# Optimization experiments

Hardware: AMD Instinct MI355X
Metric: run time of the kernel (lower is better)

The kernel has to match this reference:

```python
import jax, jax.numpy as jnp
import numpy as np

T, B, F, H, O = 512, 64, 128, 512, 16


def setup_inputs() -> dict:
    key = jax.random.key(0)
    ks = jax.random.split(key, 8)
    s = 1.0 / np.sqrt(H)  # torch RNN/Linear default uniform init scale
    u = lambda k, shape: jax.random.uniform(k, shape, jnp.float32, -s, s)
    return {
        "x_rnn": jax.random.normal(ks[0], (T, B, F), jnp.float32),
        "w_ih": u(ks[1], (3 * H, F)),   # gate order: r, z, n (PyTorch GRU)
        "w_hh": u(ks[2], (3 * H, H)),
        "b_ih": u(ks[3], (3 * H,)),
        "b_hh": u(ks[4], (3 * H,)),
        "w_out": u(ks[5], (O, H)),
        "b_out": u(ks[6], (O,)),
    }


def reference(x_rnn, w_ih, w_hh, b_ih, b_hh, w_out, b_out):
    # Single-layer GRU, seq-first (T, B, F), h0 = zeros (torch default when hx=None).
    h_dim = w_hh.shape[1]
    # Precompute all input-side gate pre-activations in one big GEMM: (T, B, 3H)
    xg = jnp.einsum("tbf,gf->tbg", x_rnn, w_ih) + b_ih

    def step(h, xg_t):
        hg = h @ w_hh.T + b_hh               # (B, 3H)
        xr, xz, xn = jnp.split(xg_t, 3, axis=-1)
        hr, hz, hn = jnp.split(hg, 3, axis=-1)
        r = jax.nn.sigmoid(xr + hr)
        z = jax.nn.sigmoid(xz + hz)
        n = jnp.tanh(xn + r * hn)
        h_new = (1.0 - z) * n + z * h
        return h_new, h_new

    h0 = jnp.zeros((x_rnn.shape[1], h_dim), x_rnn.dtype)
    _, hs = jax.lax.scan(step, h0, xg)       # hs: (T, B, H)
    # Output projection y = hs @ W_out^T + b_out -> (T, B, O)
    return jnp.einsum("tbh,oh->tbo", hs, w_out) + b_out
```

## Files before the change

### kernel.cpp

```cpp
#include <hip/hip_runtime.h>
#include <stdint.h>
#include <stddef.h>


#define T_LEN 512
#define B_SZ  64
#define F_DIM 128
#define H_DIM 512
#define O_DIM 16
#define SENTINEL 0xAAAAAAAAu

typedef __attribute__((ext_vector_type(8))) short short8;
typedef __attribute__((ext_vector_type(4))) float floatx4;
typedef __attribute__((ext_vector_type(2))) float floatx2;
typedef __attribute__((ext_vector_type(4))) unsigned int uintx4;

__device__ __forceinline__ unsigned short f2bf(float f) {
  unsigned u = __builtin_bit_cast(unsigned, f);
  u += 0x7fffu + ((u >> 16) & 1u);
  return (unsigned short)(u >> 16);
}

__device__ __forceinline__ float sigmoidf_(float x) {
  return 1.0f / (1.0f + __expf(-x));
}

__device__ __forceinline__ float tanhf_(float x) {
  float v = fminf(fmaxf(x, -10.f), 10.f);
  float e = __expf(2.f * v);
  return (e - 1.f) / (e + 1.f);
}

__device__ __forceinline__ short8 cvt8(floatx4 f0, floatx4 f1) {
  short8 a;
  a[0] = (short)f2bf(f0[0]); a[1] = (short)f2bf(f0[1]);
  a[2] = (short)f2bf(f0[2]); a[3] = (short)f2bf(f0[3]);
  a[4] = (short)f2bf(f1[0]); a[5] = (short)f2bf(f1[1]);
  a[6] = (short)f2bf(f1[2]); a[7] = (short)f2bf(f1[3]);
  return a;
}

__device__ __forceinline__ void hload4_sc1(floatx4* hf, const unsigned short* hbase) {
  asm volatile(
      "global_load_dwordx4 %0, %4, off sc1\n\t"
      "global_load_dwordx4 %1, %4, off offset:64 sc1\n\t"
      "global_load_dwordx4 %2, %4, off offset:128 sc1\n\t"
      "global_load_dwordx4 %3, %4, off offset:192 sc1\n\t"
      "s_waitcnt vmcnt(0)"
      : "=&v"(hf[0]), "=&v"(hf[1]), "=&v"(hf[2]), "=&v"(hf[3])
      : "v"(hbase)
      : "memory");
}

__global__ __launch_bounds__(256, 1)
void gru_persistent(const float* __restrict__ x,
                    const float* __restrict__ w_ih,
                    const float* __restrict__ w_hh,
                    const float* __restrict__ b_ih,
                    const float* __restrict__ b_hh,
                    unsigned short* __restrict__ hs) {
  __shared__ float part[2][4][4][16][33];

  const int tid  = threadIdx.x;
  const int lane = tid & 63;
  const int wv   = tid >> 6;
  const int bg   = blockIdx.x >> 4;
  const int cg   = blockIdx.x & 15;
  const int bgbase  = bg * 16;
  const int colbase = cg * 32;
  const int n16  = lane & 15;
  const int quad = lane >> 4;

  short8 bwx[3][2];
  short8 bwh[3][2][4];
  #pragma unroll
  for (int g = 0; g < 3; ++g) {
    #pragma unroll
    for (int nt = 0; nt < 2; ++nt) {
      const int grow = g * H_DIM + colbase + nt * 16 + n16;
      const float* pih = w_ih + (size_t)grow * F_DIM + wv * 32 + quad * 8;
      {
        short8 v;
        #pragma unroll
        for (int j = 0; j < 8; ++j) v[j] = (short)f2bf(pih[j]);
        bwx[g][nt] = v;
      }
      const float* phh = w_hh + (size_t)grow * H_DIM + wv * 128 + quad * 8;
      #pragma unroll
      for (int i = 0; i < 4; ++i) {
        short8 v;
        #pragma unroll
        for (int j = 0; j < 8; ++j) v[j] = (short)f2bf(phh[i * 32 + j]);
        bwh[g][nt][i] = v;
      }
    }
  }

  const int ew_b  = tid >> 4;
  const int ew_j0 = (tid & 15) * 2;
  float b_rz[2], b_zz[2], b_in[2], b_hn[2];
  #pragma unroll
  for (int e = 0; e < 2; ++e) {
    const int c = colbase + ew_j0 + e;
    b_rz[e] = b_ih[c] + b_hh[c];
    b_zz[e] = b_ih[H_DIM + c] + b_hh[H_DIM + c];
    b_in[e] = b_ih[2 * H_DIM + c];
    b_hn[e] = b_hh[2 * H_DIM + c];
  }
  float hm[2] = {0.0f, 0.0f};

  floatx4 xf0, xf1;
  {
    const float* px = x + ((size_t)(bgbase + n16)) * F_DIM + wv * 32 + quad * 8;
    xf0 = *(const floatx4*)px;
    xf1 = *(const floatx4*)(px + 4);
  }

  int mguard = 1 << 18;

  for (int t = 0; t < T_LEN; ++t) {
    floatx4 aR0 = {0.f,0.f,0.f,0.f}, aR1 = {0.f,0.f,0.f,0.f};
    floatx4 aZ0 = {0.f,0.f,0.f,0.f}, aZ1 = {0.f,0.f,0.f,0.f};
    floatx4 aX0 = {0.f,0.f,0.f,0.f}, aX1 = {0.f,0.f,0.f,0.f};
    floatx4 aH0 = {0.f,0.f,0.f,0.f}, aH1 = {0.f,0.f,0.f,0.f};
    {
      short8 a = cvt8(xf0, xf1);
      aR0 = __builtin_amdgcn_mfma_f32_16x16x32_bf16(a, bwx[0][0], aR0, 0, 0, 0);
      aR1 = __builtin_amdgcn_mfma_f32_16x16x32_bf16(a, bwx[0][1], aR1, 0, 0, 0);
      aZ0 = __builtin_amdgcn_mfma_f32_16x16x32_bf16(a, bwx[1][0], aZ0, 0, 0, 0);
      aZ1 = __builtin_amdgcn_mfma_f32_16x16x32_bf16(a, bwx[1][1], aZ1, 0, 0, 0);
      aX0 = __builtin_amdgcn_mfma_f32_16x16x32_bf16(a, bwx[2][0], aX0, 0, 0, 0);
      aX1 = __builtin_amdgcn_mfma_f32_16x16x32_bf16(a, bwx[2][1], aX1, 0, 0, 0);
    }

    if (t > 0) {
      floatx4 hf[4];
      {
        const unsigned short* hbase =
            hs + ((size_t)((t - 1) * B_SZ + bgbase + n16)) * H_DIM + wv * 128 + quad * 8;
        while (true) {
          hload4_sc1(hf, hbase);
          bool ok = true;
          #pragma unroll
          for (int i = 0; i < 4; ++i) {
            uintx4 u = __builtin_bit_cast(uintx4, hf[i]);
            ok = ok && (u[0] != SENTINEL) && (u[1] != SENTINEL) &&
                       (u[2] != SENTINEL) && (u[3] != SENTINEL);
          }
          if (__ballot(!ok) == 0ull) break;
          if (--mguard <= 0) break;
        }
      }
      if (t + 1 < T_LEN) {
        const float* px = x + ((size_t)((t + 1) * B_SZ + bgbase + n16)) * F_DIM +
                          wv * 32 + quad * 8;
        xf0 = *(const floatx4*)px;
        xf1 = *(const floatx4*)(px + 4);
      }
      #pragma unroll
      for (int i = 0; i < 4; ++i) {
        short8 a = __builtin_bit_cast(short8, hf[i]);
        aR0 = __builtin_amdgcn_mfma_f32_16x16x32_bf16(a, bwh[0][0][i], aR0, 0, 0, 0);
        aR1 = __builtin_amdgcn_mfma_f32_16x16x32_bf16(a, bwh[0][1][i], aR1, 0, 0, 0);
        aZ0 = __builtin_amdgcn_mfma_f32_16x16x32_bf16(a, bwh[1][0][i], aZ0, 0, 0, 0);
        aZ1 = __builtin_amdgcn_mfma_f32_16x16x32_bf16(a, bwh[1][1][i], aZ1, 0, 0, 0);
        aH0 = __builtin_amdgcn_mfma_f32_16x16x32_bf16(a, bwh[2][0][i], aH0, 0, 0, 0);
        aH1 = __builtin_amdgcn_mfma_f32_16x16x32_bf16(a, bwh[2][1][i], aH1, 0, 0, 0);
      }
    } else {
      const float* px = x + ((size_t)(B_SZ + bgbase + n16)) * F_DIM + wv * 32 + quad * 8;
      xf0 = *(const floatx4*)px;
      xf1 = *(const floatx4*)(px + 4);
    }

    {
      const int tb = t & 1;
      #pragma unroll
      for (int i = 0; i < 4; ++i) {
        const int r = quad * 4 + i;
        part[tb][wv][0][r][n16]      = aR0[i];
        part[tb][wv][0][r][16 + n16] = aR1[i];
        part[tb][wv][1][r][n16]      = aZ0[i];
        part[tb][wv][1][r][16 + n16] = aZ1[i];
        part[tb][wv][2][r][n16]      = aX0[i];
        part[tb][wv][2][r][16 + n16] = aX1[i];
        part[tb][wv][3][r][n16]      = aH0[i];
        part[tb][wv][3][r][16 + n16] = aH1[i];
      }
    }
    __syncthreads();

    {
      const int tb = t & 1;
      floatx2 pr = {0.f, 0.f}, pz = {0.f, 0.f}, pxn = {0.f, 0.f}, ph = {0.f, 0.f};
      #pragma unroll
      for (int w = 0; w < 4; ++w) {
        pr  += *(const floatx2*)&part[tb][w][0][ew_b][ew_j0];
        pz  += *(const floatx2*)&part[tb][w][1][ew_b][ew_j0];
        pxn += *(const floatx2*)&part[tb][w][2][ew_b][ew_j0];
        ph  += *(const floatx2*)&part[tb][w][3][ew_b][ew_j0];
      }
      unsigned short hb[2];
      #pragma unroll
      for (int e = 0; e < 2; ++e) {
        const float r = sigmoidf_(pr[e] + b_rz[e]);
        const float z = sigmoidf_(pz[e] + b_zz[e]);
        const float n = tanhf_(pxn[e] + b_in[e] + r * (ph[e] + b_hn[e]));
        const float hn2 = (1.0f - z) * n + z * hm[e];
        hm[e] = hn2;
        hb[e] = f2bf(hn2);
      }
      const unsigned int packed = ((unsigned int)hb[1] << 16) | (unsigned int)hb[0];
      unsigned int* dst = (unsigned int*)(hs +
          ((size_t)(t * B_SZ + bgbase + ew_b)) * H_DIM + colbase + ew_j0);
      __hip_atomic_store(dst, packed, __ATOMIC_RELAXED, __HIP_MEMORY_SCOPE_AGENT);
    }
  }
}

__global__ __launch_bounds__(256, 1)
void gru_proj(const unsigned short* __restrict__ hs,
              const float* __restrict__ w_out,
              const float* __restrict__ b_out,
              float* __restrict__ y) {
  const int tid  = threadIdx.x;
  const int lane = tid & 63;
  const int wv   = tid >> 6;
  const int n16  = lane & 15;
  const int quad = lane >> 4;
  const size_t rowbase = ((size_t)blockIdx.x * 4 + wv) * 16;

  short8 bw[16];
  const float* pw = w_out + (size_t)n16 * H_DIM + quad * 8;
  #pragma unroll
  for (int kc = 0; kc < 16; ++kc) {
    short8 v;
    #pragma unroll
    for (int j = 0; j < 8; ++j) v[j] = (short)f2bf(pw[kc * 32 + j]);
    bw[kc] = v;
  }
  const float bo = b_out[n16];

  const unsigned short* hbase = hs + (rowbase + n16) * H_DIM + quad * 8;
  floatx4 acc = {0.f, 0.f, 0.f, 0.f};
  #pragma unroll
  for (int kc = 0; kc < 16; ++kc) {
    short8 a = *(const short8*)(hbase + kc * 32);
    acc = __builtin_amdgcn_mfma_f32_16x16x32_bf16(a, bw[kc], acc, 0, 0, 0);
  }
  #pragma unroll
  for (int i = 0; i < 4; ++i) {
    const size_t r = rowbase + quad * 4 + i;
    y[r * O_DIM + n16] = acc[i] + bo;
  }
}

extern "C" void kernel_launch(void* const* d_in, const int* in_sizes, int n_in,
                              void* d_out, int out_size, void* d_ws, size_t ws_size,
                              hipStream_t stream) {
  (void)in_sizes; (void)n_in; (void)out_size; (void)ws_size;
  const float* x     = (const float*)d_in[0];
  const float* w_ih  = (const float*)d_in[1];
  const float* w_hh  = (const float*)d_in[2];
  const float* b_ih  = (const float*)d_in[3];
  const float* b_hh  = (const float*)d_in[4];
  const float* w_out = (const float*)d_in[5];
  const float* b_out = (const float*)d_in[6];
  float* y = (float*)d_out;

  unsigned short* hs = (unsigned short*)d_ws;

  gru_persistent<<<64, 256, 0, stream>>>(x, w_ih, w_hh, b_ih, b_hh, hs);
  gru_proj<<<(T_LEN * B_SZ) / 16 / 4, 256, 0, stream>>>(hs, w_out, b_out, y);
}
```

Measured before the change: 1.136 ms.

## Fuse output projection into persistent GRU kernel with concurrent consumer blocks

Merges the recurrence and output projection into one launch: 64 blocks run the GRU recurrence while 64 extra blocks poll hs for finished timesteps and apply the projection concurrently, removing the second kernel launch and its serialized tail. The recurrent loop is restructured so h loads are issued before the input-side MFMAs to hide latency, the partial-sum LDS layout is changed to interleave gates for vector reads, and divisions are replaced with rcp plus a Newton step. This relies on sentinel-based polling and on all 128 blocks being co-resident, and consumer polling adds memory traffic.

```diff
diff --git a/kernel.cpp b/kernel.cpp
--- a/kernel.cpp
+++ b/kernel.cpp
@@ -12,8 +12,9 @@
 
 typedef __attribute__((ext_vector_type(8))) short short8;
 typedef __attribute__((ext_vector_type(4))) float floatx4;
-typedef __attribute__((ext_vector_type(2))) float floatx2;
 typedef __attribute__((ext_vector_type(4))) unsigned int uintx4;
+
+#define MFMA16(a, b, c) __builtin_amdgcn_mfma_f32_16x16x32_bf16((a), (b), (c), 0, 0, 0)
 
 __device__ __forceinline__ unsigned short f2bf(float f) {
   unsigned u = __builtin_bit_cast(unsigned, f);
@@ -21,14 +22,19 @@
   return (unsigned short)(u >> 16);
 }
 
+__device__ __forceinline__ float fastrcp(float d) {
+  float r = __builtin_amdgcn_rcpf(d);
+  return r * (2.0f - d * r);
+}
+
 __device__ __forceinline__ float sigmoidf_(float x) {
-  return 1.0f / (1.0f + __expf(-x));
+  return fastrcp(1.0f + __expf(-x));
 }
 
 __device__ __forceinline__ float tanhf_(float x) {
   float v = fminf(fmaxf(x, -10.f), 10.f);
   float e = __expf(2.f * v);
-  return (e - 1.f) / (e + 1.f);
+  return (e - 1.f) * fastrcp(e + 1.f);
 }
 
 __device__ __forceinline__ short8 cvt8(floatx4 f0, floatx4 f1) {
@@ -38,6 +44,17 @@
   a[4] = (short)f2bf(f1[0]); a[5] = (short)f2bf(f1[1]);
   a[6] = (short)f2bf(f1[2]); a[7] = (short)f2bf(f1[3]);
   return a;
+}
+
+__device__ __forceinline__ void hissue4(floatx4* hf, const unsigned short* hbase) {
+  asm volatile(
+      "global_load_dwordx4 %0, %4, off sc1\n\t"
+      "global_load_dwordx4 %1, %4, off offset:64 sc1\n\t"
+      "global_load_dwordx4 %2, %4, off offset:128 sc1\n\t"
+      "global_load_dwordx4 %3, %4, off offset:192 sc1"
+      : "=&v"(hf[0]), "=&v"(hf[1]), "=&v"(hf[2]), "=&v"(hf[3])
+      : "v"(hbase)
+      : "memory");
 }
 
 __device__ __forceinline__ void hload4_sc1(floatx4* hf, const unsigned short* hbase) {
@@ -52,206 +69,254 @@
       : "memory");
 }
 
+__device__ __forceinline__ bool clean4(const floatx4* hf) {
+  bool ok = true;
+  #pragma unroll
+  for (int i = 0; i < 4; ++i) {
+    uintx4 u = __builtin_bit_cast(uintx4, hf[i]);
+    ok = ok & (u[0] != SENTINEL) & (u[1] != SENTINEL) &
+         (u[2] != SENTINEL) & (u[3] != SENTINEL);
+  }
+  return __ballot(!ok) == 0ull;
+}
+
 __global__ __launch_bounds__(256, 1)
-void gru_persistent(const float* __restrict__ x,
-                    const float* __restrict__ w_ih,
-                    const float* __restrict__ w_hh,
-                    const float* __restrict__ b_ih,
-                    const float* __restrict__ b_hh,
-                    unsigned short* __restrict__ hs) {
-  __shared__ float part[2][4][4][16][33];
-
-  const int tid  = threadIdx.x;
-  const int lane = tid & 63;
-  const int wv   = tid >> 6;
-  const int bg   = blockIdx.x >> 4;
-  const int cg   = blockIdx.x & 15;
-  const int bgbase  = bg * 16;
-  const int colbase = cg * 32;
-  const int n16  = lane & 15;
-  const int quad = lane >> 4;
-
-  short8 bwx[3][2];
-  short8 bwh[3][2][4];
-  #pragma unroll
-  for (int g = 0; g < 3; ++g) {
-    #pragma unroll
-    for (int nt = 0; nt < 2; ++nt) {
-      const int grow = g * H_DIM + colbase + nt * 16 + n16;
-      const float* pih = w_ih + (size_t)grow * F_DIM + wv * 32 + quad * 8;
-      {
-        short8 v;
-        #pragma unroll
-        for (int j = 0; j < 8; ++j) v[j] = (short)f2bf(pih[j]);
-        bwx[g][nt] = v;
-      }
-      const float* phh = w_hh + (size_t)grow * H_DIM + wv * 128 + quad * 8;
-      #pragma unroll
-      for (int i = 0; i < 4; ++i) {
-        short8 v;
-        #pragma unroll
-        for (int j = 0; j < 8; ++j) v[j] = (short)f2bf(phh[i * 32 + j]);
-        bwh[g][nt][i] = v;
-      }
-    }
-  }
-
-  const int ew_b  = tid >> 4;
-  const int ew_j0 = (tid & 15) * 2;
-  float b_rz[2], b_zz[2], b_in[2], b_hn[2];
-  #pragma unroll
-  for (int e = 0; e < 2; ++e) {
-    const int c = colbase + ew_j0 + e;
-    b_rz[e] = b_ih[c] + b_hh[c];
-    b_zz[e] = b_ih[H_DIM + c] + b_hh[H_DIM + c];
-    b_in[e] = b_ih[2 * H_DIM + c];
-    b_hn[e] = b_hh[2 * H_DIM + c];
-  }
-  float hm[2] = {0.0f, 0.0f};
-
-  floatx4 xf0, xf1;
-  {
-    const float* px = x + ((size_t)(bgbase + n16)) * F_DIM + wv * 32 + quad * 8;
-    xf0 = *(const floatx4*)px;
-    xf1 = *(const floatx4*)(px + 4);
-  }
-
-  int mguard = 1 << 18;
-
-  for (int t = 0; t < T_LEN; ++t) {
-    floatx4 aR0 = {0.f,0.f,0.f,0.f}, aR1 = {0.f,0.f,0.f,0.f};
-    floatx4 aZ0 = {0.f,0.f,0.f,0.f}, aZ1 = {0.f,0.f,0.f,0.f};
-    floatx4 aX0 = {0.f,0.f,0.f,0.f}, aX1 = {0.f,0.f,0.f,0.f};
-    floatx4 aH0 = {0.f,0.f,0.f,0.f}, aH1 = {0.f,0.f,0.f,0.f};
-    {
-      short8 a = cvt8(xf0, xf1);
-      aR0 = __builtin_amdgcn_mfma_f32_16x16x32_bf16(a, bwx[0][0], aR0, 0, 0, 0);
-      aR1 = __builtin_amdgcn_mfma_f32_16x16x32_bf16(a, bwx[0][1], aR1, 0, 0, 0);
-      aZ0 = __builtin_amdgcn_mfma_f32_16x16x32_bf16(a, bwx[1][0], aZ0, 0, 0, 0);
-      aZ1 = __builtin_amdgcn_mfma_f32_16x16x32_bf16(a, bwx[1][1], aZ1, 0, 0, 0);
-      aX0 = __builtin_amdgcn_mfma_f32_16x16x32_bf16(a, bwx[2][0], aX0, 0, 0, 0);
-      aX1 = __builtin_amdgcn_mfma_f32_16x16x32_bf16(a, bwx[2][1], aX1, 0, 0, 0);
-    }
-
-    if (t > 0) {
-      floatx4 hf[4];
-      {
-        const unsigned short* hbase =
-            hs + ((size_t)((t - 1) * B_SZ + bgbase + n16)) * H_DIM + wv * 128 + quad * 8;
-        while (true) {
-          hload4_sc1(hf, hbase);
-          bool ok = true;
-          #pragma unroll
-          for (int i = 0; i < 4; ++i) {
-            uintx4 u = __builtin_bit_cast(uintx4, hf[i]);
-            ok = ok && (u[0] != SENTINEL) && (u[1] != SENTINEL) &&
-                       (u[2] != SENTINEL) && (u[3] != SENTINEL);
-          }
-          if (__ballot(!ok) == 0ull) break;
-          if (--mguard <= 0) break;
-        }
-      }
-      if (t + 1 < T_LEN) {
-        const float* px = x + ((size_t)((t + 1) * B_SZ + bgbase + n16)) * F_DIM +
-                          wv * 32 + quad * 8;
-        xf0 = *(const floatx4*)px;
-        xf1 = *(const floatx4*)(px + 4);
-      }
-      #pragma unroll
-      for (int i = 0; i < 4; ++i) {
-        short8 a = __builtin_bit_cast(short8, hf[i]);
-        aR0 = __builtin_amdgcn_mfma_f32_16x16x32_bf16(a, bwh[0][0][i], aR0, 0, 0, 0);
-        aR1 = __builtin_amdgcn_mfma_f32_16x16x32_bf16(a, bwh[0][1][i], aR1, 0, 0, 0);
-        aZ0 = __builtin_amdgcn_mfma_f32_16x16x32_bf16(a, bwh[1][0][i], aZ0, 0, 0, 0);
-        aZ1 = __builtin_amdgcn_mfma_f32_16x16x32_bf16(a, bwh[1][1][i], aZ1, 0, 0, 0);
-        aH0 = __builtin_amdgcn_mfma_f32_16x16x32_bf16(a, bwh[2][0][i], aH0, 0, 0, 0);
-        aH1 = __builtin_amdgcn_mfma_f32_16x16x32_bf16(a, bwh[2][1][i], aH1, 0, 0, 0);
-      }
-    } else {
-      const float* px = x + ((size_t)(B_SZ + bgbase + n16)) * F_DIM + wv * 32 + quad * 8;
-      xf0 = *(const floatx4*)px;
-      xf1 = *(const floatx4*)(px + 4);
-    }
-
-    {
-      const int tb = t & 1;
-      #pragma unroll
-      for (int i = 0; i < 4; ++i) {
-        const int r = quad * 4 + i;
-        part[tb][wv][0][r][n16]      = aR0[i];
-        part[tb][wv][0][r][16 + n16] = aR1[i];
-        part[tb][wv][1][r][n16]      = aZ0[i];
-        part[tb][wv][1][r][16 + n16] = aZ1[i];
-        part[tb][wv][2][r][n16]      = aX0[i];
-        part[tb][wv][2][r][16 + n16] = aX1[i];
-        part[tb][wv][3][r][n16]      = aH0[i];
-        part[tb][wv][3][r][16 + n16] = aH1[i];
-      }
-    }
-    __syncthreads();
-
-    {
-      const int tb = t & 1;
-      floatx2 pr = {0.f, 0.f}, pz = {0.f, 0.f}, pxn = {0.f, 0.f}, ph = {0.f, 0.f};
-      #pragma unroll
-      for (int w = 0; w < 4; ++w) {
-        pr  += *(const floatx2*)&part[tb][w][0][ew_b][ew_j0];
-        pz  += *(const floatx2*)&part[tb][w][1][ew_b][ew_j0];
-        pxn += *(const floatx2*)&part[tb][w][2][ew_b][ew_j0];
-        ph  += *(const floatx2*)&part[tb][w][3][ew_b][ew_j0];
-      }
-      unsigned short hb[2];
-      #pragma unroll
-      for (int e = 0; e < 2; ++e) {
-        const float r = sigmoidf_(pr[e] + b_rz[e]);
-        const float z = sigmoidf_(pz[e] + b_zz[e]);
-        const float n = tanhf_(pxn[e] + b_in[e] + r * (ph[e] + b_hn[e]));
-        const float hn2 = (1.0f - z) * n + z * hm[e];
-        hm[e] = hn2;
-        hb[e] = f2bf(hn2);
-      }
-      const unsigned int packed = ((unsigned int)hb[1] << 16) | (unsigned int)hb[0];
-      unsigned int* dst = (unsigned int*)(hs +
-          ((size_t)(t * B_SZ + bgbase + ew_b)) * H_DIM + colbase + ew_j0);
-      __hip_atomic_store(dst, packed, __ATOMIC_RELAXED, __HIP_MEMORY_SCOPE_AGENT);
-    }
-  }
-}
-
-__global__ __launch_bounds__(256, 1)
-void gru_proj(const unsigned short* __restrict__ hs,
-              const float* __restrict__ w_out,
-              const float* __restrict__ b_out,
-              float* __restrict__ y) {
+void gru_fused(const float* __restrict__ x,
+               const float* __restrict__ w_ih,
+               const float* __restrict__ w_hh,
+               const float* __restrict__ b_ih,
+               const float* __restrict__ b_hh,
+               const float* __restrict__ w_out,
+               const float* __restrict__ b_out,
+               unsigned short* __restrict__ hs,
+               float* __restrict__ y) {
+  __shared__ __align__(16) float part[2][4][16][33][4];
+
   const int tid  = threadIdx.x;
   const int lane = tid & 63;
   const int wv   = tid >> 6;
   const int n16  = lane & 15;
   const int quad = lane >> 4;
-  const size_t rowbase = ((size_t)blockIdx.x * 4 + wv) * 16;
-
-  short8 bw[16];
-  const float* pw = w_out + (size_t)n16 * H_DIM + quad * 8;
-  #pragma unroll
-  for (int kc = 0; kc < 16; ++kc) {
-    short8 v;
+  const floatx4 fzero = {0.f, 0.f, 0.f, 0.f};
+
+  if (blockIdx.x < 64) {
+    const int bg      = blockIdx.x >> 4;
+    const int cg      = blockIdx.x & 15;
+    const int bgbase  = bg * 16;
+    const int colbase = cg * 32;
+
+    short8 bwx[3][2];
+    short8 bwh[3][2][4];
     #pragma unroll
-    for (int j = 0; j < 8; ++j) v[j] = (short)f2bf(pw[kc * 32 + j]);
-    bw[kc] = v;
-  }
-  const float bo = b_out[n16];
-
-  const unsigned short* hbase = hs + (rowbase + n16) * H_DIM + quad * 8;
-  floatx4 acc = {0.f, 0.f, 0.f, 0.f};
-  #pragma unroll
-  for (int kc = 0; kc < 16; ++kc) {
-    short8 a = *(const short8*)(hbase + kc * 32);
-    acc = __builtin_amdgcn_mfma_f32_16x16x32_bf16(a, bw[kc], acc, 0, 0, 0);
-  }
-  #pragma unroll
-  for (int i = 0; i < 4; ++i) {
-    const size_t r = rowbase + quad * 4 + i;
-    y[r * O_DIM + n16] = acc[i] + bo;
+    for (int g = 0; g < 3; ++g) {
+      #pragma unroll
+      for (int nt = 0; nt < 2; ++nt) {
+        const int grow = g * H_DIM + colbase + nt * 16 + n16;
+        const float* pih = w_ih + (size_t)grow * F_DIM + wv * 32 + quad * 8;
+        {
+          short8 v;
+          #pragma unroll
+          for (int j = 0; j < 8; ++j) v[j] = (short)f2bf(pih[j]);
+          bwx[g][nt] = v;
+        }
+        const float* phh = w_hh + (size_t)grow * H_DIM + wv * 128 + quad * 8;
+        #pragma unroll
+        for (int i = 0; i < 4; ++i) {
+          short8 v;
+          #pragma unroll
+          for (int j = 0; j < 8; ++j) v[j] = (short)f2bf(phh[i * 32 + j]);
+          bwh[g][nt][i] = v;
+        }
+      }
+    }
+
+    const int ew_b  = tid >> 4;
+    const int ew_j0 = (tid & 15) * 2;
+    float b_rz[2], b_zz[2], b_in[2], b_hn[2];
+    #pragma unroll
+    for (int e = 0; e < 2; ++e) {
+      const int c = colbase + ew_j0 + e;
+      b_rz[e] = b_ih[c] + b_hh[c];
+      b_zz[e] = b_ih[H_DIM + c] + b_hh[H_DIM + c];
+      b_in[e] = b_ih[2 * H_DIM + c];
+      b_hn[e] = b_hh[2 * H_DIM + c];
+    }
+    float hm[2] = {0.0f, 0.0f};
+
+    floatx4 xf0, xf1;
+    {
+      const float* px = x + ((size_t)(bgbase + n16)) * F_DIM + wv * 32 + quad * 8;
+      xf0 = *(const floatx4*)px;
+      xf1 = *(const floatx4*)(px + 4);
+    }
+    short8 a_x = cvt8(xf0, xf1);
+
+    floatx4 aR0, aR1, aZ0, aZ1, aX0, aX1, aH0, aH1;
+    floatx4 hf[4] = {fzero, fzero, fzero, fzero};
+    int mguard = 1 << 18;
+
+    auto epilogue = [&](int t) {
+      const int tb = t & 1;
+      #pragma unroll
+      for (int i = 0; i < 4; ++i) {
+        const int r = quad * 4 + i;
+        floatx4 v0 = {aR0[i], aZ0[i], aX0[i], aH0[i]};
+        floatx4 v1 = {aR1[i], aZ1[i], aX1[i], aH1[i]};
+        *(floatx4*)&part[tb][wv][r][n16][0]      = v0;
+        *(floatx4*)&part[tb][wv][r][16 + n16][0] = v1;
+      }
+      __syncthreads();
+      if (t + 1 < T_LEN) a_x = cvt8(xf0, xf1);
+      float pr[2] = {0.f, 0.f}, pz[2] = {0.f, 0.f};
+      float pn[2] = {0.f, 0.f}, ph[2] = {0.f, 0.f};
+      #pragma unroll
+      for (int w = 0; w < 4; ++w) {
+        #pragma unroll
+        for (int e = 0; e < 2; ++e) {
+          floatx4 g = *(const floatx4*)&part[tb][w][ew_b][ew_j0 + e][0];
+          pr[e] += g[0]; pz[e] += g[1]; pn[e] += g[2]; ph[e] += g[3];
+        }
+      }
+      unsigned short hb2[2];
+      #pragma unroll
+      for (int e = 0; e < 2; ++e) {
+        const float r = sigmoidf_(pr[e] + b_rz[e]);
+        const float z = sigmoidf_(pz[e] + b_zz[e]);
+        const float n = tanhf_(pn[e] + b_in[e] + r * (ph[e] + b_hn[e]));
+        const float hn2 = (1.0f - z) * n + z * hm[e];
+        hm[e] = hn2;
+        hb2[e] = f2bf(hn2);
+      }
+      const unsigned int packed = ((unsigned int)hb2[1] << 16) | (unsigned int)hb2[0];
+      unsigned int* dst = (unsigned int*)(hs +
+          ((size_t)(t * B_SZ + bgbase + ew_b)) * H_DIM + colbase + ew_j0);
+      __hip_atomic_store(dst, packed, __ATOMIC_RELAXED, __HIP_MEMORY_SCOPE_AGENT);
+    };
+
+    {
+      aR0 = MFMA16(a_x, bwx[0][0], fzero); aR1 = MFMA16(a_x, bwx[0][1], fzero);
+      aZ0 = MFMA16(a_x, bwx[1][0], fzero); aZ1 = MFMA16(a_x, bwx[1][1], fzero);
+      aX0 = MFMA16(a_x, bwx[2][0], fzero); aX1 = MFMA16(a_x, bwx[2][1], fzero);
+      aH0 = fzero; aH1 = fzero;
+      {
+        const float* pxn = x + ((size_t)(B_SZ + bgbase + n16)) * F_DIM + wv * 32 + quad * 8;
+        asm volatile("global_load_dwordx4 %0, %2, off\n\t"
+                     "global_load_dwordx4 %1, %2, off offset:16"
+                     : "=&v"(xf0), "=&v"(xf1) : "v"(pxn) : "memory");
+      }
+      asm volatile("s_waitcnt vmcnt(0)" ::: "memory");
+      __builtin_amdgcn_sched_barrier(0);
+      epilogue(0);
+    }
+
+    for (int t = 1; t < T_LEN; ++t) {
+      const unsigned short* hbase =
+          hs + ((size_t)((t - 1) * B_SZ + bgbase + n16)) * H_DIM + wv * 128 + quad * 8;
+
+      hissue4(hf, hbase);
+      __builtin_amdgcn_sched_barrier(0);
+
+      aR0 = MFMA16(a_x, bwx[0][0], fzero); aR1 = MFMA16(a_x, bwx[0][1], fzero);
+      aZ0 = MFMA16(a_x, bwx[1][0], fzero); aZ1 = MFMA16(a_x, bwx[1][1], fzero);
+      aX0 = MFMA16(a_x, bwx[2][0], fzero); aX1 = MFMA16(a_x, bwx[2][1], fzero);
+      aH0 = fzero; aH1 = fzero;
+
+      asm volatile("s_waitcnt vmcnt(0)" ::: "memory");
+      __builtin_amdgcn_sched_barrier(0);
+
+      while (!clean4(hf)) {
+        if (--mguard <= 0) break;
+        hload4_sc1(hf, hbase);
+      }
+
+      if (t + 1 < T_LEN) {
+        const float* pxn = x + ((size_t)((t + 1) * B_SZ + bgbase + n16)) * F_DIM +
+                           wv * 32 + quad * 8;
+        asm volatile("global_load_dwordx4 %0, %2, off\n\t"
+                     "global_load_dwordx4 %1, %2, off offset:16"
+                     : "=&v"(xf0), "=&v"(xf1) : "v"(pxn) : "memory");
+      }
+
+      #pragma unroll
+      for (int i = 0; i < 4; ++i) {
+        short8 a = __builtin_bit_cast(short8, hf[i]);
+        aR0 = MFMA16(a, bwh[0][0][i], aR0); aR1 = MFMA16(a, bwh[0][1][i], aR1);
+        aZ0 = MFMA16(a, bwh[1][0][i], aZ0); aZ1 = MFMA16(a, bwh[1][1][i], aZ1);
+        aH0 = MFMA16(a, bwh[2][0][i], aH0); aH1 = MFMA16(a, bwh[2][1][i], aH1);
+      }
+
+      __builtin_amdgcn_sched_barrier(0);
+      asm volatile("s_waitcnt vmcnt(0)" ::: "memory");
+      __builtin_amdgcn_sched_barrier(0);
+
+      epilogue(t);
+    }
+  } else {
+    const int p = (int)blockIdx.x - 64;
+
+    short8 bw[16];
+    const float* pw = w_out + (size_t)n16 * H_DIM + quad * 8;
+    #pragma unroll
+    for (int kc = 0; kc < 16; ++kc) {
+      short8 v;
+      #pragma unroll
+      for (int j = 0; j < 8; ++j) v[j] = (short)f2bf(pw[kc * 32 + j]);
+      bw[kc] = v;
+    }
+    const float bo = b_out[n16];
+
+    int sguard = 1 << 12;
+    int fguard = 1 << 10;
+
+    for (int k = 0; k < 8; ++k) {
+      const int t = p * 8 + k;
+      const size_t rowb = (size_t)t * B_SZ + wv * 16;
+
+      {
+        const int srow = lane & 15;
+        const int scg  = ((lane >> 4) * 4 + (srow & 3)) & 15;
+        const unsigned short* sp = hs + (rowb + srow) * H_DIM + scg * 32 + 12;
+        while (true) {
+          unsigned int sv;
+          asm volatile("global_load_dword %0, %1, off sc1\n\t"
+                       "s_waitcnt vmcnt(0)"
+                       : "=&v"(sv) : "v"(sp) : "memory");
+          __builtin_amdgcn_sched_barrier(0);
+          if (__ballot(sv == SENTINEL) == 0ull) break;
+          if (--sguard <= 0) break;
+          __builtin_amdgcn_s_sleep(48);
+        }
+      }
+
+      floatx4 hv[16];
+      const unsigned short* hb = hs + (rowb + n16) * H_DIM + quad * 8;
+      while (true) {
+        #pragma unroll
+        for (int g = 0; g < 4; ++g) hissue4(&hv[4 * g], hb + g * 128);
+        asm volatile("s_waitcnt vmcnt(0)" ::: "memory");
+        __builtin_amdgcn_sched_barrier(0);
+        bool ok = true;
+        #pragma unroll
+        for (int i = 0; i < 16; ++i) {
+          uintx4 u = __builtin_bit_cast(uintx4, hv[i]);
+          ok = ok & (u[0] != SENTINEL) & (u[1] != SENTINEL) &
+               (u[2] != SENTINEL) & (u[3] != SENTINEL);
+        }
+        if (__ballot(!ok) == 0ull) break;
+        if (--fguard <= 0) break;
+        __builtin_amdgcn_s_sleep(8);
+      }
+
+      floatx4 acc = fzero;
+      #pragma unroll
+      for (int kc = 0; kc < 16; ++kc)
+        acc = MFMA16(__builtin_bit_cast(short8, hv[kc]), bw[kc], acc);
+      #pragma unroll
+      for (int i = 0; i < 4; ++i) {
+        const size_t r = rowb + quad * 4 + i;
+        y[r * O_DIM + n16] = acc[i] + bo;
+      }
+    }
   }
 }
 
@@ -270,6 +335,5 @@
 
   unsigned short* hs = (unsigned short*)d_ws;
 
-  gru_persistent<<<64, 256, 0, stream>>>(x, w_ih, w_hh, b_ih, b_hh, hs);
-  gru_proj<<<(T_LEN * B_SZ) / 16 / 4, 256, 0, stream>>>(hs, w_out, b_out, y);
-}
+  gru_fused<<<128, 256, 0, stream>>>(x, w_ih, w_hh, b_ih, b_hh, w_out, b_out, hs, y);
+}
```

New measurement: 1.410 ms. +24.1%, slower.
